# Kernel optimization log

Hardware: AMD Instinct MI355X
Metric: run time of the kernel (lower is better)

## Reference

```python
import jax, jax.numpy as jnp
import numpy as np

N_NODES = 50000
N_EDGES = 800000
D = 64


def setup_inputs() -> dict:
    key = jax.random.key(0)
    k1, k2, k3, k4, k5, k6, k7 = jax.random.split(key, 7)
    h = jax.random.normal(k1, (N_NODES, D), dtype=jnp.float32)
    x = jax.random.normal(k2, (N_NODES, 3), dtype=jnp.float32)
    edge_index = jax.random.randint(k3, (2, N_EDGES), 0, N_NODES, dtype=jnp.int64)
    # fc_h: Linear(D, D); fc_x: Linear(D, 1). PyTorch default init scale ~1/sqrt(fan_in).
    s = 1.0 / np.sqrt(D)
    W_h = jax.random.uniform(k4, (D, D), minval=-s, maxval=s, dtype=jnp.float32)
    b_h = jax.random.uniform(k5, (D,), minval=-s, maxval=s, dtype=jnp.float32)
    W_x = jax.random.uniform(k6, (D, 1), minval=-s, maxval=s, dtype=jnp.float32)
    b_x = jax.random.uniform(k7, (1,), minval=-s, maxval=s, dtype=jnp.float32)
    return {"h": h, "x": x, "edge_index": edge_index,
            "W_h": W_h, "b_h": b_h, "W_x": W_x, "b_x": b_x}


def reference(h, x, edge_index, W_h, b_h, W_x, b_x):
    row, col = edge_index[0], edge_index[1]
    h_j = h[col]                                   # [E, D] gather
    delta_x = x[row] - x[col]                      # [E, 3]
    m = jax.nn.relu(h_j @ W_h + b_h)               # [E, D]
    agg_h = jax.ops.segment_sum(m, row, num_segments=h.shape[0])
    h_new = h + agg_h
    weight = jax.nn.relu(h_j @ W_x + b_x)          # [E, 1]
    agg_x = jax.ops.segment_sum(delta_x * weight, row, num_segments=x.shape[0])
    x_new = x + agg_x
    return (h_new, x_new)
```

## Files before the change

### kernel.cpp

```cpp
#include <hip/hip_runtime.h>
#include <hip/hip_fp16.h>

#define N_NODES 50000
#define N_EDGES 800000
#define D 64
#define BLOCK 256

#define NBIN 256
#define BINW 196
#define BCAP 3584
#define EPB 4096
#define NBINBLK 196
#define PREBLK 196
#define SUBS 8
#define RNODES 25
#define QCAP 576
#define ROWS_PS 2

__global__ __launch_bounds__(BLOCK) void pre_bin_kernel(
    const float* __restrict__ h, const float* __restrict__ x,
    const int* __restrict__ eidx,
    const float* __restrict__ Wh, const float* __restrict__ bh,
    const float* __restrict__ Wx, const float* __restrict__ bx,
    __half2* __restrict__ M16, float4* __restrict__ px,
    int* __restrict__ bins, int* __restrict__ gcur) {
  const unsigned b = blockIdx.x;

  if (b < NBINBLK) {
    __shared__ int cnt[NBIN], ssc[NBIN], start[NBIN], cur[NBIN], gbase[NBIN];
    __shared__ int stage[EPB];
    const int t = threadIdx.x;
    cnt[t] = 0;
    __syncthreads();
    const int base = (int)b * EPB;
#pragma unroll 4
    for (int k = 0; k < EPB / BLOCK; ++k) {
      int e = base + k * BLOCK + t;
      if (e < N_EDGES) {
        int row = eidx[e];
        if ((unsigned)row < N_NODES) atomicAdd(&cnt[row / BINW], 1);
      }
    }
    __syncthreads();
    ssc[t] = cnt[t];
    __syncthreads();
    for (int off = 1; off < NBIN; off <<= 1) {
      int v = (t >= off) ? ssc[t - off] : 0;
      __syncthreads();
      ssc[t] += v;
      __syncthreads();
    }
    int ex = ssc[t] - cnt[t];
    start[t] = ex;
    cur[t] = ex;
    gbase[t] = cnt[t] ? atomicAdd(&gcur[t], cnt[t]) : 0;
    __syncthreads();
#pragma unroll 4
    for (int k = 0; k < EPB / BLOCK; ++k) {
      int e = base + k * BLOCK + t;
      if (e < N_EDGES) {
        int row = eidx[e];
        int col = eidx[N_EDGES + e];
        if ((unsigned)row < N_NODES && (unsigned)col < N_NODES) {
          int bb = row / BINW;
          int pos = atomicAdd(&cur[bb], 1);
          stage[pos] = (bb << 24) | ((row - bb * BINW) << 16) | col;
        }
      }
    }
    __syncthreads();
    const int total = ssc[NBIN - 1];
    for (int idx = t; idx < total; idx += BLOCK) {
      int e = stage[idx];
      int bb = ((unsigned)e) >> 24;
      int dst = gbase[bb] + (idx - start[bb]);
      if (dst < BCAP) bins[(size_t)bb * BCAP + dst] = e;
    }
    return;
  }

  const int pid = (int)b - NBINBLK;
  const int i = pid * BLOCK + threadIdx.x;
  if (i >= N_NODES) return;

  const float4* __restrict__ h4 = (const float4*)(h + (size_t)i * D);
  const float4* __restrict__ Wx4 = (const float4*)Wx;

  float acc[D];
#pragma unroll
  for (int d = 0; d < D; ++d) acc[d] = bh[d];
  float wx = bx[0];

  for (int q = 0; q < D / 4; ++q) {
    float4 hv = h4[q];
    float4 wxv = Wx4[q];
    wx = fmaf(hv.x, wxv.x, fmaf(hv.y, wxv.y, fmaf(hv.z, wxv.z,
         fmaf(hv.w, wxv.w, wx))));
#pragma unroll
    for (int r = 0; r < 4; ++r) {
      float hk = (r == 0) ? hv.x : (r == 1) ? hv.y : (r == 2) ? hv.z : hv.w;
      const float4* wr4 = (const float4*)(Wh + (q * 4 + r) * D);
#pragma unroll
      for (int dq = 0; dq < D / 4; ++dq) {
        float4 wv = wr4[dq];
        acc[4 * dq + 0] = fmaf(hk, wv.x, acc[4 * dq + 0]);
        acc[4 * dq + 1] = fmaf(hk, wv.y, acc[4 * dq + 1]);
        acc[4 * dq + 2] = fmaf(hk, wv.z, acc[4 * dq + 2]);
        acc[4 * dq + 3] = fmaf(hk, wv.w, acc[4 * dq + 3]);
      }
    }
  }

  __half2 hh[D / 2];
#pragma unroll
  for (int j = 0; j < D / 2; ++j)
    hh[j] = __floats2half2_rn(fmaxf(acc[2 * j], 0.0f),
                              fmaxf(acc[2 * j + 1], 0.0f));
  float4* mrow = (float4*)(M16 + (size_t)i * 32);
  const float4* hhp = (const float4*)hh;
#pragma unroll
  for (int q = 0; q < 8; ++q) mrow[q] = hhp[q];

  float w = fmaxf(wx, 0.0f);
  px[i] = make_float4(w, w * x[(size_t)i * 3 + 0],
                      w * x[(size_t)i * 3 + 1],
                      w * x[(size_t)i * 3 + 2]);
}

__global__ __launch_bounds__(256, 8) void agg_kernel(
    const float* __restrict__ h, const float* __restrict__ x,
    const int* __restrict__ bins, const int* __restrict__ gcur,
    const __half2* __restrict__ M16, const float4* __restrict__ px,
    float* __restrict__ out) {
  __shared__ int stage2[BCAP];
  __shared__ int qs[QCAP];
  __shared__ int hist[RNODES], rcur[RNODES];
  __shared__ int rstart[RNODES + 1];

  const int t = threadIdx.x;
  const int bin = blockIdx.x >> 3, sub = blockIdx.x & 7;
  const int lbase = sub * RNODES;
  const int gb = bin * BINW + lbase;
  const int R = min(min(RNODES, BINW - lbase), N_NODES - gb);
  if (R <= 0) return;

  if (t < RNODES) hist[t] = 0;
  __syncthreads();

  const int n = min(gcur[bin], BCAP);
  const int* bs = bins + (size_t)bin * BCAP;
  for (int i = t; i < n; i += 256) {
    int e = bs[i];
    stage2[i] = e;
    unsigned dd = (unsigned)((e >> 16) & 0xff) - (unsigned)lbase;
    if (dd < (unsigned)R) atomicAdd(&hist[dd], 1);
  }
  __syncthreads();
  if (t < 64) {
    int myh = (t < R) ? hist[t] : 0;
    int v = myh;
#pragma unroll
    for (int off = 1; off < 64; off <<= 1) {
      int u = __shfl_up(v, off);
      if (t >= off) v += u;
    }
    if (t == 0) rstart[0] = 0;
    if (t < R) { rstart[t + 1] = v; rcur[t] = v - myh; }
  }
  __syncthreads();
  for (int i = t; i < n; i += 256) {
    int e = stage2[i];
    unsigned dd = (unsigned)((e >> 16) & 0xff) - (unsigned)lbase;
    if (dd < (unsigned)R) {
      int pos = atomicAdd(&rcur[dd], 1);
      if (pos < QCAP) qs[pos] = e;
    }
  }
  __syncthreads();

  const float* pxf = (const float*)px;
  const float2* M2 = (const float2*)M16;
  const int l16 = t & 15;
  const int stream = t >> 4;
  const int wbase = t & 48;
  const size_t xb = (size_t)N_NODES * D;

  float ac[ROWS_PS][4];
  float ps[ROWS_PS];
#pragma unroll
  for (int k = 0; k < ROWS_PS; ++k) {
    ac[k][0] = ac[k][1] = ac[k][2] = ac[k][3] = 0.f;
    ps[k] = 0.f;
  }

#pragma unroll
  for (int k = 0; k < ROWS_PS; ++k) {
    int rr = stream + 16 * k;
    if (rr < R) {
      int beg = min(rstart[rr], QCAP);
      int end = min(rstart[rr + 1], QCAP);
      for (int qi = beg; qi < end; qi += 8) {
        float2 g[8];
        float pv[8];
        bool val[8];
        int cs[8];
#pragma unroll
        for (int j = 0; j < 8; ++j) {
          int idx = qi + j;
          val[j] = idx < end;
          int e = qs[val[j] ? idx : beg];
          cs[j] = e & 0xffff;
          if (val[j]) g[j] = M2[(size_t)cs[j] * 16 + l16];
        }
#pragma unroll
        for (int j = 0; j < 8; ++j) {
          pv[j] = 0.f;
          if (val[j] && l16 < 4) pv[j] = pxf[cs[j] * 4 + l16];
        }
#pragma unroll
        for (int j = 0; j < 8; ++j)
          if (val[j]) {
            const __half2* hp = (const __half2*)&g[j];
            float2 f0 = __half22float2(hp[0]);
            float2 f1 = __half22float2(hp[1]);
            ac[k][0] += f0.x; ac[k][1] += f0.y;
            ac[k][2] += f1.x; ac[k][3] += f1.y;
            ps[k] += pv[j];
          }
      }
    }
  }

#pragma unroll
  for (int k = 0; k < ROWS_PS; ++k) {
    int rr = stream + 16 * k;
    if (rr < R) {
      int gn = gb + rr;
      float4 hvv = ((const float4*)h)[(size_t)gn * 16 + l16];
      ((float4*)out)[(size_t)gn * 16 + l16] =
          make_float4(hvv.x + ac[k][0], hvv.y + ac[k][1],
                      hvv.z + ac[k][2], hvv.w + ac[k][3]);
      float W = __shfl(ps[k], wbase);
      float pc = __shfl(ps[k], wbase + l16 + 1);
      if (l16 < 3)
        out[xb + (size_t)gn * 3 + l16] =
            fmaf(x[(size_t)gn * 3 + l16], 1.0f + W, -pc);
    }
  }
}


__global__ __launch_bounds__(256) void init_out_kernel(
    const float* __restrict__ h, const float* __restrict__ x,
    float* __restrict__ out) {
  const int NH4 = N_NODES * D / 4;
  const int NT4 = (N_NODES * D + N_NODES * 3) / 4;
  int i = blockIdx.x * 256 + threadIdx.x;
  if (i >= NT4) return;
  float4 v;
  if (i < NH4) v = ((const float4*)h)[i];
  else         v = ((const float4*)x)[i - NH4];
  ((float4*)out)[i] = v;
}

__global__ __launch_bounds__(256) void edge_kernel(
    const float* __restrict__ h, const float* __restrict__ x,
    const int* __restrict__ eidx,
    const float* __restrict__ Wh, const float* __restrict__ bh,
    const float* __restrict__ Wx, const float* __restrict__ bx,
    float* __restrict__ out) {
  int e = blockIdx.x * 256 + threadIdx.x;
  if (e >= N_EDGES) return;
  int row = eidx[e];
  int col = eidx[N_EDGES + e];
  if ((unsigned)row >= N_NODES || (unsigned)col >= N_NODES) return;
  const float* hj = h + (size_t)col * D;
  float acc[D];
#pragma unroll
  for (int dd = 0; dd < D; ++dd) acc[dd] = bh[dd];
  float wsum = bx[0];
#pragma unroll 2
  for (int kg = 0; kg < D / 4; ++kg) {
    float4 hv = *(const float4*)(hj + kg * 4);
#pragma unroll
    for (int j = 0; j < 4; ++j) {
      float hk = (j == 0) ? hv.x : (j == 1) ? hv.y : (j == 2) ? hv.z : hv.w;
      int k = kg * 4 + j;
      wsum = fmaf(hk, Wx[k], wsum);
      const float* wrow = Wh + k * D;
#pragma unroll
      for (int dd = 0; dd < D; ++dd) acc[dd] = fmaf(hk, wrow[dd], acc[dd]);
    }
  }
  float* outh = out + (size_t)row * D;
#pragma unroll
  for (int dd = 0; dd < D; ++dd) atomicAdd(&outh[dd], fmaxf(acc[dd], 0.0f));
  float w = fmaxf(wsum, 0.0f);
  float* outx = out + (size_t)N_NODES * D + (size_t)row * 3;
  const float* xr = x + (size_t)row * 3;
  const float* xc = x + (size_t)col * 3;
#pragma unroll
  for (int c = 0; c < 3; ++c) atomicAdd(&outx[c], (xr[c] - xc[c]) * w);
}


extern "C" void kernel_launch(void* const* d_in, const int* in_sizes, int n_in,
                              void* d_out, int out_size, void* d_ws, size_t ws_size,
                              hipStream_t stream) {
  const float* h    = (const float*)d_in[0];
  const float* x    = (const float*)d_in[1];
  const int*   eidx = (const int*)d_in[2];
  const float* Wh   = (const float*)d_in[3];
  const float* bh   = (const float*)d_in[4];
  const float* Wx   = (const float*)d_in[5];
  const float* bx   = (const float*)d_in[6];
  float* out = (float*)d_out;

  size_t need = (size_t)N_NODES * D * 2 + (size_t)N_NODES * 16 +
                (size_t)NBIN * BCAP * 4 + 1024;

  if (ws_size < need) {
    const int NT4 = (N_NODES * D + N_NODES * 3) / 4;
    init_out_kernel<<<(NT4 + 255) / 256, 256, 0, stream>>>(h, x, out);
    edge_kernel<<<(N_EDGES + 255) / 256, 256, 0, stream>>>(
        h, x, eidx, Wh, bh, Wx, bx, out);
    return;
  }

  __half2* M16 = (__half2*)d_ws;
  float4*  px  = (float4*)((char*)d_ws + (size_t)N_NODES * D * 2);
  int*     bins = (int*)((char*)px + (size_t)N_NODES * 16);
  int*     gcur = bins + (size_t)NBIN * BCAP;

  hipMemsetAsync(gcur, 0, NBIN * sizeof(int), stream);
  pre_bin_kernel<<<NBINBLK + PREBLK, BLOCK, 0, stream>>>(
      h, x, eidx, Wh, bh, Wx, bx, M16, px, bins, gcur);
  agg_kernel<<<NBIN * SUBS, 256, 0, stream>>>(
      h, x, bins, gcur, M16, px, out);
}
```

Baseline: 127.9 us.

## Cache edge indices in registers, use nontemporal loads/stores, shrink gather depth

The binning phase now loads each thread's 16 row/col indices once into registers and reuses them for both the histogram and the scatter pass, instead of reading the edge index array twice. Streaming accesses (edge indices, bin writes and reads, h/x reads, output writes) use nontemporal builtins so they do not displace the gathered message table in cache. The aggregation gather depth drops from 8 to 6 loads in flight, which lowers register pressure but also reduces memory-level parallelism. The register arrays raise register use in the pre-bin kernel.

Measured after the change: 132.9 us. 4.0% more time.

```diff
diff --git a/kernel.cpp b/kernel.cpp
--- a/kernel.cpp
+++ b/kernel.cpp
@@ -10,12 +10,19 @@
 #define BINW 196
 #define BCAP 3584
 #define EPB 4096
+#define KIT 16
 #define NBINBLK 196
 #define PREBLK 196
 #define SUBS 8
 #define RNODES 25
 #define QCAP 576
 #define ROWS_PS 2
+#define DEPTH 6
+
+typedef float vf4 __attribute__((ext_vector_type(4)));
+
+#define NTL(p)    __builtin_nontemporal_load(p)
+#define NTS(v, p) __builtin_nontemporal_store(v, p)
 
 __global__ __launch_bounds__(BLOCK) void pre_bin_kernel(
     const float* __restrict__ h, const float* __restrict__ x,
@@ -33,14 +40,24 @@
     cnt[t] = 0;
     __syncthreads();
     const int base = (int)b * EPB;
-#pragma unroll 4
-    for (int k = 0; k < EPB / BLOCK; ++k) {
+    int rows[KIT], cols[KIT];
+#pragma unroll
+    for (int k = 0; k < KIT; ++k) {
       int e = base + k * BLOCK + t;
+      rows[k] = -1;
+      cols[k] = 0;
       if (e < N_EDGES) {
-        int row = eidx[e];
-        if ((unsigned)row < N_NODES) atomicAdd(&cnt[row / BINW], 1);
-      }
-    }
+        int row = NTL(eidx + e);
+        int col = NTL(eidx + N_EDGES + e);
+        if ((unsigned)row < N_NODES && (unsigned)col < N_NODES) {
+          rows[k] = row;
+          cols[k] = col;
+        }
+      }
+    }
+#pragma unroll
+    for (int k = 0; k < KIT; ++k)
+      if (rows[k] >= 0) atomicAdd(&cnt[rows[k] / BINW], 1);
     __syncthreads();
     ssc[t] = cnt[t];
     __syncthreads();
@@ -55,17 +72,12 @@
     cur[t] = ex;
     gbase[t] = cnt[t] ? atomicAdd(&gcur[t], cnt[t]) : 0;
     __syncthreads();
-#pragma unroll 4
-    for (int k = 0; k < EPB / BLOCK; ++k) {
-      int e = base + k * BLOCK + t;
-      if (e < N_EDGES) {
-        int row = eidx[e];
-        int col = eidx[N_EDGES + e];
-        if ((unsigned)row < N_NODES && (unsigned)col < N_NODES) {
-          int bb = row / BINW;
-          int pos = atomicAdd(&cur[bb], 1);
-          stage[pos] = (bb << 24) | ((row - bb * BINW) << 16) | col;
-        }
+#pragma unroll
+    for (int k = 0; k < KIT; ++k) {
+      if (rows[k] >= 0) {
+        int bb = rows[k] / BINW;
+        int pos = atomicAdd(&cur[bb], 1);
+        stage[pos] = (bb << 24) | ((rows[k] - bb * BINW) << 16) | cols[k];
       }
     }
     __syncthreads();
@@ -74,7 +86,7 @@
       int e = stage[idx];
       int bb = ((unsigned)e) >> 24;
       int dst = gbase[bb] + (idx - start[bb]);
-      if (dst < BCAP) bins[(size_t)bb * BCAP + dst] = e;
+      if (dst < BCAP) NTS(e, bins + (size_t)bb * BCAP + dst);
     }
     return;
   }
@@ -150,7 +162,7 @@
   const int n = min(gcur[bin], BCAP);
   const int* bs = bins + (size_t)bin * BCAP;
   for (int i = t; i < n; i += 256) {
-    int e = bs[i];
+    int e = NTL(bs + i);
     stage2[i] = e;
     unsigned dd = (unsigned)((e >> 16) & 0xff) - (unsigned)lbase;
     if (dd < (unsigned)R) atomicAdd(&hist[dd], 1);
@@ -199,13 +211,13 @@
     if (rr < R) {
       int beg = min(rstart[rr], QCAP);
       int end = min(rstart[rr + 1], QCAP);
-      for (int qi = beg; qi < end; qi += 8) {
-        float2 g[8];
-        float pv[8];
-        bool val[8];
-        int cs[8];
-#pragma unroll
-        for (int j = 0; j < 8; ++j) {
+      for (int qi = beg; qi < end; qi += DEPTH) {
+        float2 g[DEPTH];
+        float pv[DEPTH];
+        bool val[DEPTH];
+        int cs[DEPTH];
+#pragma unroll
+        for (int j = 0; j < DEPTH; ++j) {
           int idx = qi + j;
           val[j] = idx < end;
           int e = qs[val[j] ? idx : beg];
@@ -213,12 +225,12 @@
           if (val[j]) g[j] = M2[(size_t)cs[j] * 16 + l16];
         }
 #pragma unroll
-        for (int j = 0; j < 8; ++j) {
+        for (int j = 0; j < DEPTH; ++j) {
           pv[j] = 0.f;
           if (val[j] && l16 < 4) pv[j] = pxf[cs[j] * 4 + l16];
         }
 #pragma unroll
-        for (int j = 0; j < 8; ++j)
+        for (int j = 0; j < DEPTH; ++j)
           if (val[j]) {
             const __half2* hp = (const __half2*)&g[j];
             float2 f0 = __half22float2(hp[0]);
@@ -236,15 +248,17 @@
     int rr = stream + 16 * k;
     if (rr < R) {
       int gn = gb + rr;
-      float4 hvv = ((const float4*)h)[(size_t)gn * 16 + l16];
-      ((float4*)out)[(size_t)gn * 16 + l16] =
-          make_float4(hvv.x + ac[k][0], hvv.y + ac[k][1],
-                      hvv.z + ac[k][2], hvv.w + ac[k][3]);
+      vf4 hvv = NTL(((const vf4*)h) + (size_t)gn * 16 + l16);
+      vf4 ov;
+      ov.x = hvv.x + ac[k][0]; ov.y = hvv.y + ac[k][1];
+      ov.z = hvv.z + ac[k][2]; ov.w = hvv.w + ac[k][3];
+      NTS(ov, ((vf4*)out) + (size_t)gn * 16 + l16);
       float W = __shfl(ps[k], wbase);
       float pc = __shfl(ps[k], wbase + l16 + 1);
-      if (l16 < 3)
-        out[xb + (size_t)gn * 3 + l16] =
-            fmaf(x[(size_t)gn * 3 + l16], 1.0f + W, -pc);
+      if (l16 < 3) {
+        float xv = NTL(x + (size_t)gn * 3 + l16);
+        NTS(fmaf(xv, 1.0f + W, -pc), out + xb + (size_t)gn * 3 + l16);
+      }
     }
   }
 }
@@ -332,7 +346,7 @@
   int*     bins = (int*)((char*)px + (size_t)N_NODES * 16);
   int*     gcur = bins + (size_t)NBIN * BCAP;
 
-  hipMemsetAsync(gcur, 0, NBIN * sizeof(int), stream);
+  (void)hipMemsetAsync(gcur, 0, NBIN * sizeof(int), stream);
   pre_bin_kernel<<<NBINBLK + PREBLK, BLOCK, 0, stream>>>(
       h, x, eidx, Wh, bh, Wx, bx, M16, px, bins, gcur);
   agg_kernel<<<NBIN * SUBS, 256, 0, stream>>>(
```
